# Performance work log

Hardware: AMD Instinct MI355X
Metric: run time of the kernel (lower is better)

The kernel has to match this reference:

```python
import jax, jax.numpy as jnp
import numpy as np

B, T, D, H, L, INNER = 2, 2048, 1024, 16, 8, 4096
EPS = 1e-5
MASK_BIAS = -10000.0

def setup_inputs() -> dict:
    key = jax.random.key(0)
    ks = jax.random.split(key, 6)
    std = 0.02
    w = lambda k, shape: jax.random.normal(k, shape, jnp.float32) * std
    return {
        "inputs_embeds": jax.random.normal(ks[0], (B, T, D), jnp.float32),
        "attention_mask": jnp.ones((B, T), jnp.float32),
        "ln1_w": jnp.ones((L, D), jnp.float32), "ln1_b": jnp.zeros((L, D), jnp.float32),
        "attn_w": w(ks[1], (L, D, 3 * D)), "attn_b": jnp.zeros((L, 3 * D), jnp.float32),
        "proj_w": w(ks[2], (L, D, D)), "proj_b": jnp.zeros((L, D), jnp.float32),
        "ln2_w": jnp.ones((L, D), jnp.float32), "ln2_b": jnp.zeros((L, D), jnp.float32),
        "fc_w": w(ks[3], (L, D, INNER)), "fc_b": jnp.zeros((L, INNER), jnp.float32),
        "fcp_w": w(ks[4], (L, INNER, D)), "fcp_b": jnp.zeros((L, D), jnp.float32),
        "lnf_w": jnp.ones((D,), jnp.float32), "lnf_b": jnp.zeros((D,), jnp.float32),
    }

def _ln(x, w, b):
    m = jnp.mean(x, axis=-1, keepdims=True)
    v = jnp.var(x, axis=-1, keepdims=True)
    return (x - m) * jax.lax.rsqrt(v + EPS) * w + b

def reference(inputs_embeds, attention_mask, ln1_w, ln1_b, attn_w, attn_b,
              proj_w, proj_b, ln2_w, ln2_b, fc_w, fc_b, fcp_w, fcp_b,
              lnf_w, lnf_b):
    hd = D // H
    scale = 1.0 / np.sqrt(hd).astype(np.float32)
    causal = jnp.tril(jnp.ones((T, T), bool))            # [T,T]
    add_mask = (1.0 - attention_mask)[:, None, None, :] * MASK_BIAS  # [B,1,1,T]
    heads = lambda t: t.reshape(B, T, H, hd).transpose(0, 2, 1, 3)   # [B,H,T,hd]
    h = inputs_embeds  # dropout is identity at eval
    for i in range(L):
        # --- causal self-attention (manual QK^T / softmax / AV) ---
        x = _ln(h, ln1_w[i], ln1_b[i])
        qkv = x @ attn_w[i] + attn_b[i]                  # [B,T,3D]
        q, k, v = (heads(t) for t in jnp.split(qkv, 3, axis=-1))
        s = jnp.einsum('bhqd,bhkd->bhqk', q, k) * scale  # [B,H,T,T]
        s = jnp.where(causal, s, MASK_BIAS) + add_mask   # masked_fill then additive mask
        p = jax.nn.softmax(s, axis=-1)
        ctx = jnp.einsum('bhqk,bhkd->bhqd', p, v)
        ctx = ctx.transpose(0, 2, 1, 3).reshape(B, T, D)
        h = h + ctx @ proj_w[i] + proj_b[i]
        # --- feed-forward ---
        x = _ln(h, ln2_w[i], ln2_b[i])
        h = h + jax.nn.relu(x @ fc_w[i] + fc_b[i]) @ fcp_w[i] + fcp_b[i]
    return _ln(h, lnf_w, lnf_b)
```

## Files before the change

### kernel.cpp

```cpp
#include <hip/hip_runtime.h>
#include <math.h>

namespace {
constexpr int kB = 2;
constexpr int kT = 2048;
constexpr int kD = 1024;
constexpr int kH = 16;
constexpr int kL = 8;
constexpr int kInner = 4096;
constexpr int kM = kB * kT;
constexpr float kEps = 1e-5f;
}

typedef __attribute__((ext_vector_type(8))) short bf16x8;
typedef __attribute__((ext_vector_type(4))) float f32x4;
typedef __attribute__((ext_vector_type(16))) float f32x16;

typedef const __attribute__((address_space(1))) void* gas_t;
typedef __attribute__((address_space(3))) void* las_t;

__device__ __forceinline__ short f2bf(float f) {
  union { float f; unsigned u; } v{f};
  unsigned r = (v.u + 0x7FFF + ((v.u >> 16) & 1)) >> 16;
  return (short)r;
}

__device__ __forceinline__ unsigned cvtpk_bf16(float lo, float hi) {
  unsigned r;
  asm("v_cvt_pk_bf16_f32 %0, %1, %2" : "=v"(r) : "v"(lo), "v"(hi));
  return r;
}

__device__ __forceinline__ void half_swap(unsigned& a, unsigned& b, bool ishi) {
  const unsigned sel = ishi ? a : b;
  const unsigned got = (unsigned)__shfl_xor((int)sel, 32, 64);
  a = ishi ? got : a;
  b = ishi ? b : got;
}

template <typename OT>
__global__ __launch_bounds__(256) void ln_kernel(
    const float* __restrict__ in, const float* __restrict__ w,
    const float* __restrict__ b, OT* __restrict__ out) {
  const int row = blockIdx.x;
  const int tid = threadIdx.x;
  const float4 v = ((const float4*)(in + (size_t)row * kD))[tid];
  float sum = v.x + v.y + v.z + v.w;
  float sq = v.x * v.x + v.y * v.y + v.z * v.z + v.w * v.w;
#pragma unroll
  for (int off = 32; off > 0; off >>= 1) {
    sum += __shfl_down(sum, off);
    sq += __shfl_down(sq, off);
  }
  __shared__ float s1[4], s2[4];
  const int wave = tid >> 6, lane = tid & 63;
  if (lane == 0) { s1[wave] = sum; s2[wave] = sq; }
  __syncthreads();
  const float ts = s1[0] + s1[1] + s1[2] + s1[3];
  const float tq = s2[0] + s2[1] + s2[2] + s2[3];
  const float mean = ts * (1.0f / kD);
  const float var = tq * (1.0f / kD) - mean * mean;
  const float rs = rsqrtf(var + kEps);
  const float4 w4 = ((const float4*)w)[tid];
  const float4 b4 = ((const float4*)b)[tid];
  float4 o;
  o.x = (v.x - mean) * rs * w4.x + b4.x;
  o.y = (v.y - mean) * rs * w4.y + b4.y;
  o.z = (v.z - mean) * rs * w4.z + b4.z;
  o.w = (v.w - mean) * rs * w4.w + b4.w;
  if constexpr (sizeof(OT) == 4) {
    ((float4*)(out + (size_t)row * kD))[tid] = o;
  } else {
    short4 s4;
    s4.x = f2bf(o.x); s4.y = f2bf(o.y); s4.z = f2bf(o.z); s4.w = f2bf(o.w);
    ((short4*)(out + (size_t)row * kD))[tid] = s4;
  }
}

__global__ __launch_bounds__(256) void convT_kernel(
    const float* __restrict__ aw, const float* __restrict__ pw,
    const float* __restrict__ fw, const float* __restrict__ gw,
    short* __restrict__ awT, short* __restrict__ pwT,
    short* __restrict__ fwT, short* __restrict__ gwT) {
  __shared__ short t[64][66];
  int b = blockIdx.x;
  const float* src; short* dst; int K, N, tk, tn;
  if (b < 768)       { src = aw; dst = awT; K = 1024; N = 3072; tk = b / 48; tn = b % 48; }
  else if (b < 1024) { b -= 768;  src = pw; dst = pwT; K = 1024; N = 1024; tk = b / 16; tn = b % 16; }
  else if (b < 2048) { b -= 1024; src = fw; dst = fwT; K = 1024; N = 4096; tk = b / 64; tn = b % 64; }
  else               { b -= 2048; src = gw; dst = gwT; K = 4096; N = 1024; tk = b / 16; tn = b % 16; }
  const int k0 = tk * 64, n0 = tn * 64;
  const int tr = threadIdx.x >> 4, tc4 = (threadIdx.x & 15) << 2;
#pragma unroll
  for (int i = 0; i < 4; ++i) {
    const int k = tr + i * 16;
    const float4 v = *(const float4*)(src + (size_t)(k0 + k) * N + n0 + tc4);
    t[k][tc4 + 0] = f2bf(v.x); t[k][tc4 + 1] = f2bf(v.y);
    t[k][tc4 + 2] = f2bf(v.z); t[k][tc4 + 3] = f2bf(v.w);
  }
  __syncthreads();
#pragma unroll
  for (int i = 0; i < 4; ++i) {
    const int n = tr + i * 16;
    short4 o;
    o.x = t[tc4 + 0][n]; o.y = t[tc4 + 1][n];
    o.z = t[tc4 + 2][n]; o.w = t[tc4 + 3][n];
    *(short4*)(dst + (size_t)(n0 + n) * K + k0 + tc4) = o;
  }
}

template <int OUT, bool RELU>
__global__ __launch_bounds__(256, 2) void mfma_gemm3(
    const short* __restrict__ A, const short* __restrict__ BT,
    const float* __restrict__ bias, const float* __restrict__ res,
    void* __restrict__ Cout, int N, int K) {
  __shared__ __align__(16) short As[2][128 * 64];
  __shared__ __align__(16) short Bs[2][128 * 64];
  const int tid = threadIdx.x;
  const int w = tid >> 6, lane = tid & 63;
  const int n16 = lane & 15, quad = lane >> 4;
  const int gridN = N >> 7;
  int bid = blockIdx.x;
  const int nwg = gridDim.x;
  bid = (bid & 7) * (nwg >> 3) + (bid >> 3);
  const int m0 = (bid / gridN) * 128, n0 = (bid % gridN) * 128;
  const int wr = (w >> 1) * 64, wc = (w & 1) * 64;

  const short* Ap = A + (size_t)m0 * K;
  const short* Bp = BT + (size_t)n0 * K;

  f32x4 acc[4][4];
#pragma unroll
  for (int i = 0; i < 4; ++i)
#pragma unroll
    for (int j = 0; j < 4; ++j) acc[i][j] = (f32x4)0.f;

  const int srow = tid >> 3;
  const int schunk = tid & 7;

  auto STAGE = [&](int buf, int k0) {
#pragma unroll
    for (int i = 0; i < 4; ++i) {
      const int r = i * 32 + srow;
      const int cs = (schunk ^ (r & 7)) << 3;
      __builtin_amdgcn_global_load_lds(
          (gas_t)(const void*)(Ap + (size_t)r * K + k0 + cs),
          (las_t)(void*)(As[buf] + (i * 32 + w * 8) * 64), 16, 0, 0);
      __builtin_amdgcn_global_load_lds(
          (gas_t)(const void*)(Bp + (size_t)r * K + k0 + cs),
          (las_t)(void*)(Bs[buf] + (i * 32 + w * 8) * 64), 16, 0, 0);
    }
  };

  STAGE(0, 0);
  __syncthreads();
  int cur = 0;

  for (int k0 = 0; k0 < K; k0 += 64) {
    if (k0 + 64 < K) STAGE(cur ^ 1, k0 + 64);
    const short* as_ = As[cur];
    const short* bs_ = Bs[cur];

    bf16x8 af[4][2], bf[4][2];
#pragma unroll
    for (int i = 0; i < 4; ++i) {
      const int m = wr + i * 16 + n16;
      const int n = wc + i * 16 + n16;
#pragma unroll
      for (int kc = 0; kc < 2; ++kc) {
        af[i][kc] =
            *(const bf16x8*)(as_ + m * 64 + ((((kc << 2) + quad) ^ (m & 7)) << 3));
        bf[i][kc] =
            *(const bf16x8*)(bs_ + n * 64 + ((((kc << 2) + quad) ^ (n & 7)) << 3));
      }
    }
    __builtin_amdgcn_s_setprio(1);
#pragma unroll
    for (int i = 0; i < 4; ++i)
#pragma unroll
      for (int j = 0; j < 4; ++j)
#pragma unroll
        for (int kc = 0; kc < 2; ++kc)
          acc[i][j] = __builtin_amdgcn_mfma_f32_16x16x32_bf16(af[i][kc], bf[j][kc],
                                                              acc[i][j], 0, 0, 0);
    __builtin_amdgcn_s_setprio(0);
    __syncthreads();
    cur ^= 1;
  }

#pragma unroll
  for (int j = 0; j < 4; ++j) {
    const int n = n0 + wc + j * 16 + n16;
    const float bv = bias[n];
#pragma unroll
    for (int i = 0; i < 4; ++i) {
#pragma unroll
      for (int r = 0; r < 4; ++r) {
        const int m = m0 + wr + i * 16 + quad * 4 + r;
        float v = acc[i][j][r] + bv;
        if (OUT == 1) {
          ((float*)Cout)[(size_t)m * N + n] = v + res[(size_t)m * N + n];
        } else {
          if (RELU) v = fmaxf(v, 0.f);
          ((short*)Cout)[(size_t)m * N + n] = f2bf(v);
        }
      }
    }
  }
}

__global__ __launch_bounds__(256) void attn_kernel(
    const short* __restrict__ qkv, const float* __restrict__ amaskp,
    short* __restrict__ ctx) {
  __shared__ __align__(16) short smem[2][8192];

  const int tid = threadIdx.x;
  const int w = tid >> 6;
  const int lane = tid & 63;
  const int l31 = lane & 31;
  const int hi = lane >> 5;
  const int bh = blockIdx.x;
  const int bb = bh >> 4, hh = bh & 15;
  const int qb = gridDim.y - 1 - blockIdx.y;
  const int q0 = qb * 128;
  const int qw0 = q0 + w * 32;

  const short* base  = qkv + (size_t)bb * kT * 3072;
  const short* kbase = base + 1024 + hh * 64;
  const short* vbase = base + 2048 + hh * 64;
  const float* amp   = amaskp + bb * kT;

  bf16x8 qf[4];
  {
    const short* qp = base + (size_t)(qw0 + l31) * 3072 + hh * 64 + hi * 8;
#pragma unroll
    for (int mi = 0; mi < 4; ++mi) qf[mi] = *(const bf16x8*)(qp + mi * 16);
  }

  f32x16 O[2];
  O[0] = (f32x16)0.f;
  O[1] = (f32x16)0.f;
  float m_r = -1e30f, l_r = 0.f;

  const int krow = tid >> 3, kch = tid & 7;
  const int vk4 = tid >> 5, vd16 = (tid >> 3) & 3;
  const int vkin = (tid >> 1) & 3, vdh = tid & 1;
  const int wuni = (tid & 192) * 8;

  const unsigned vs0 = (unsigned)(size_t)(las_t)(void*)(&smem[0][4096]);
  const int g = lane >> 4;
  const unsigned vtr =
      vs0 + (unsigned)((g >> 1) * 1024 + (g & 1) * 128 + (lane & 15) * 8);

  auto STAGE = [&](int buf, int k0) {
    short* ks = &smem[buf][0];
    short* vs = &smem[buf][4096];
#pragma unroll
    for (int r2 = 0; r2 < 2; ++r2) {
      const int rr = r2 * 32 + krow;
      __builtin_amdgcn_global_load_lds(
          (gas_t)(const void*)(kbase + (size_t)(k0 + rr) * 3072 +
                               ((kch ^ (rr & 7)) << 3)),
          (las_t)(void*)(ks + r2 * 2048 + wuni), 16, 0, 0);
      const int key = k0 + r2 * 32 + vk4 * 4 + vkin;
      __builtin_amdgcn_global_load_lds(
          (gas_t)(const void*)(vbase + (size_t)key * 3072 + vd16 * 16 + vdh * 8),
          (las_t)(void*)(vs + r2 * 2048 + wuni), 16, 0, 0);
    }
  };

  const int kend = q0 + 128;
  STAGE(0, 0);
  __syncthreads();
  int cur = 0;

  for (int k0 = 0; k0 < kend; k0 += 64) {
    if (k0 + 64 < kend) STAGE(cur ^ 1, k0 + 64);

    if (k0 <= qw0 + 31) {
      const short* ks = &smem[cur][0];

      f32x16 st[2];
      st[0] = (f32x16)0.f;
      st[1] = (f32x16)0.f;
#pragma unroll
      for (int s = 0; s < 2; ++s) {
        const int row = s * 32 + l31;
        const short* kp = ks + row * 64;
#pragma unroll
        for (int mi = 0; mi < 4; ++mi) {
          const bf16x8 kf =
              *(const bf16x8*)(kp + (((2 * mi + hi) ^ (row & 7)) << 3));
          st[s] = __builtin_amdgcn_mfma_f32_32x32x16_bf16(kf, qf[mi], st[s],
                                                          0, 0, 0);
        }
      }

#pragma unroll
      for (int s = 0; s < 2; ++s) {
        const bool pm = (k0 + 32 * s + 31 > qw0);
#pragma unroll
        for (int rq = 0; rq < 4; ++rq) {
          const int kb_ = k0 + 32 * s + 8 * rq + 4 * hi;
          const float4 a4 = *(const float4*)(amp + kb_);
          const float amv0 = (1.f - a4.x) * -10000.f;
          const float amv1 = (1.f - a4.y) * -10000.f;
          const float amv2 = (1.f - a4.z) * -10000.f;
          const float amv3 = (1.f - a4.w) * -10000.f;
          float v0 = st[s][rq * 4 + 0] * 0.125f;
          float v1 = st[s][rq * 4 + 1] * 0.125f;
          float v2 = st[s][rq * 4 + 2] * 0.125f;
          float v3 = st[s][rq * 4 + 3] * 0.125f;
          if (pm) {
            const int q = qw0 + l31;
            if (kb_ + 0 > q) v0 = -10000.f;
            if (kb_ + 1 > q) v1 = -10000.f;
            if (kb_ + 2 > q) v2 = -10000.f;
            if (kb_ + 3 > q) v3 = -10000.f;
          }
          st[s][rq * 4 + 0] = v0 + amv0;
          st[s][rq * 4 + 1] = v1 + amv1;
          st[s][rq * 4 + 2] = v2 + amv2;
          st[s][rq * 4 + 3] = v3 + amv3;
        }
      }

      float mx = st[0][0];
#pragma unroll
      for (int r = 1; r < 16; ++r) mx = fmaxf(mx, st[0][r]);
#pragma unroll
      for (int r = 0; r < 16; ++r) mx = fmaxf(mx, st[1][r]);
      mx = fmaxf(mx, __shfl_xor(mx, 32, 64));
      const float mn = fmaxf(m_r, mx);
      const float al = __expf(m_r - mn);
      m_r = mn;
      float sum = 0.f;
#pragma unroll
      for (int s = 0; s < 2; ++s)
#pragma unroll
        for (int r = 0; r < 16; ++r) {
          const float p = __expf(st[s][r] - mn);
          st[s][r] = p;
          sum += p;
        }
      sum += __shfl_xor(sum, 32, 64);
      l_r = l_r * al + sum;
#pragma unroll
      for (int r = 0; r < 16; ++r) {
        O[0][r] *= al;
        O[1][r] *= al;
      }

      bf16x8 pf[4];
      const bool ishi = (hi != 0);
#pragma unroll
      for (int s = 0; s < 2; ++s) {
#pragma unroll
        for (int hf = 0; hf < 2; ++hf) {
          unsigned wa = cvtpk_bf16(st[s][8 * hf + 0], st[s][8 * hf + 1]);
          unsigned wc = cvtpk_bf16(st[s][8 * hf + 4], st[s][8 * hf + 5]);
          half_swap(wa, wc, ishi);
          unsigned wb = cvtpk_bf16(st[s][8 * hf + 2], st[s][8 * hf + 3]);
          unsigned wd = cvtpk_bf16(st[s][8 * hf + 6], st[s][8 * hf + 7]);
          half_swap(wb, wd, ishi);
          union { unsigned u[4]; bf16x8 h; } f;
          f.u[0] = wa; f.u[1] = wb; f.u[2] = wc; f.u[3] = wd;
          pf[s * 2 + hf] = f.h;
        }
      }

      unsigned long long tv[16];
      const unsigned vb_ = vtr + (unsigned)(cur << 14);
#pragma unroll
      for (int c = 0; c < 4; ++c)
#pragma unroll
        for (int di = 0; di < 2; ++di) {
          asm volatile("ds_read_b64_tr_b16 %0, %1 offset:%2"
                       : "=v"(tv[(c * 2 + di) * 2 + 0])
                       : "v"(vb_), "n"(c * 2048 + di * 256));
          asm volatile("ds_read_b64_tr_b16 %0, %1 offset:%2"
                       : "=v"(tv[(c * 2 + di) * 2 + 1])
                       : "v"(vb_), "n"(c * 2048 + di * 256 + 512));
        }
      asm volatile("s_waitcnt lgkmcnt(0)" ::: "memory");
      __builtin_amdgcn_sched_barrier(0);
#pragma unroll
      for (int c = 0; c < 4; ++c)
#pragma unroll
        for (int di = 0; di < 2; ++di) {
          union { unsigned long long q[2]; bf16x8 h; } vf_;
          vf_.q[0] = tv[(c * 2 + di) * 2 + 0];
          vf_.q[1] = tv[(c * 2 + di) * 2 + 1];
          O[di] = __builtin_amdgcn_mfma_f32_32x32x16_bf16(vf_.h, pf[c], O[di],
                                                          0, 0, 0);
        }
    }

    __syncthreads();
    cur ^= 1;
  }

  const float inv = 1.f / l_r;
  const size_t tok = (size_t)bb * kT + qw0 + l31;
  short* cp = ctx + tok * 1024 + hh * 64 + 4 * hi;
#pragma unroll
  for (int di = 0; di < 2; ++di)
#pragma unroll
    for (int rq = 0; rq < 4; ++rq) {
      short4 o4;
      o4.x = f2bf(O[di][rq * 4 + 0] * inv);
      o4.y = f2bf(O[di][rq * 4 + 1] * inv);
      o4.z = f2bf(O[di][rq * 4 + 2] * inv);
      o4.w = f2bf(O[di][rq * 4 + 3] * inv);
      *(short4*)(cp + di * 32 + rq * 8) = o4;
    }
}

extern "C" void kernel_launch(void* const* d_in, const int* in_sizes, int n_in,
                              void* d_out, int out_size, void* d_ws, size_t ws_size,
                              hipStream_t stream) {
  const float* emb   = (const float*)d_in[0];
  const float* amask = (const float*)d_in[1];
  const float* ln1w  = (const float*)d_in[2];
  const float* ln1b  = (const float*)d_in[3];
  const float* attnw = (const float*)d_in[4];
  const float* attnb = (const float*)d_in[5];
  const float* projw = (const float*)d_in[6];
  const float* projb = (const float*)d_in[7];
  const float* ln2w  = (const float*)d_in[8];
  const float* ln2b  = (const float*)d_in[9];
  const float* fcw   = (const float*)d_in[10];
  const float* fcb   = (const float*)d_in[11];
  const float* fcpw  = (const float*)d_in[12];
  const float* fcpb  = (const float*)d_in[13];
  const float* lnfw  = (const float*)d_in[14];
  const float* lnfb  = (const float*)d_in[15];
  float* out = (float*)d_out;

  float* h    = (float*)d_ws;
  short* xb   = (short*)(h + (size_t)kM * kD);
  short* ctxb = xb + (size_t)kM * kD;
  short* bigb = ctxb + (size_t)kM * kD;
  short* awT  = bigb + (size_t)kM * kInner;
  short* pwT  = awT + (size_t)3072 * 1024;
  short* fwT  = pwT + (size_t)1024 * 1024;
  short* gwT  = fwT + (size_t)4096 * 1024;

  hipMemcpyAsync(h, emb, sizeof(float) * (size_t)kM * kD,
                 hipMemcpyDeviceToDevice, stream);

  const dim3 blk(256);
  for (int l = 0; l < kL; ++l) {
    convT_kernel<<<3072, blk, 0, stream>>>(
        attnw + (size_t)l * kD * 3072, projw + (size_t)l * kD * kD,
        fcw + (size_t)l * kD * kInner, fcpw + (size_t)l * kInner * kD,
        awT, pwT, fwT, gwT);
    ln_kernel<short><<<kM, blk, 0, stream>>>(h, ln1w + l * kD, ln1b + l * kD, xb);
    mfma_gemm3<0, false><<<(3072 / 128) * (kM / 128), blk, 0, stream>>>(
        xb, awT, attnb + l * 3072, nullptr, bigb, 3072, 1024);
    attn_kernel<<<dim3(kB * kH, kT / 128), blk, 0, stream>>>(bigb, amask, ctxb);
    mfma_gemm3<1, false><<<(1024 / 128) * (kM / 128), blk, 0, stream>>>(
        ctxb, pwT, projb + l * kD, h, h, 1024, 1024);
    ln_kernel<short><<<kM, blk, 0, stream>>>(h, ln2w + l * kD, ln2b + l * kD, xb);
    mfma_gemm3<0, true><<<(4096 / 128) * (kM / 128), blk, 0, stream>>>(
        xb, fwT, fcb + l * kInner, nullptr, bigb, 4096, 1024);
    mfma_gemm3<1, false><<<(1024 / 128) * (kM / 128), blk, 0, stream>>>(
        bigb, gwT, fcpb + l * kD, h, h, 1024, 4096);
  }
  ln_kernel<float><<<kM, blk, 0, stream>>>(h, lnfw, lnfb, out);
}
```

Measured before the change: 2.392 ms.

## Single-buffer GEMM for higher occupancy, narrow N tiles, lazy softmax rescale

The GEMM drops LDS double buffering and raises launch bounds to 4 waves per SIMD, so more blocks can be resident. It also gains a template N-tile width, and the two N=1024 GEMMs now use 64-wide tiles, which doubles their block count. In attention, the online-softmax rescale of the running max, sum and output is skipped when the new block max exceeds the old by no more than 8. This trades load/compute overlap inside a block for occupancy-based latency hiding, and the lazy rescale accepts exponentials bounded by e^8.

```diff
diff --git a/kernel.cpp b/kernel.cpp
--- a/kernel.cpp
+++ b/kernel.cpp
@@ -109,87 +109,81 @@
   }
 }
 
-template <int OUT, bool RELU>
-__global__ __launch_bounds__(256, 2) void mfma_gemm3(
+template <int BN_, int OUT, bool RELU>
+__global__ __launch_bounds__(256, 4) void mfma_gemm3(
     const short* __restrict__ A, const short* __restrict__ BT,
     const float* __restrict__ bias, const float* __restrict__ res,
     void* __restrict__ Cout, int N, int K) {
-  __shared__ __align__(16) short As[2][128 * 64];
-  __shared__ __align__(16) short Bs[2][128 * 64];
+  constexpr int NJ = BN_ / 32;
+  __shared__ __align__(16) short As[128 * 64];
+  __shared__ __align__(16) short Bs[BN_ * 64];
   const int tid = threadIdx.x;
   const int w = tid >> 6, lane = tid & 63;
   const int n16 = lane & 15, quad = lane >> 4;
-  const int gridN = N >> 7;
+  const int gridN = N / BN_;
   int bid = blockIdx.x;
   const int nwg = gridDim.x;
   bid = (bid & 7) * (nwg >> 3) + (bid >> 3);
-  const int m0 = (bid / gridN) * 128, n0 = (bid % gridN) * 128;
-  const int wr = (w >> 1) * 64, wc = (w & 1) * 64;
+  const int m0 = (bid / gridN) * 128, n0 = (bid % gridN) * BN_;
+  const int wr = (w >> 1) * 64, wc = (w & 1) * (BN_ / 2);
 
   const short* Ap = A + (size_t)m0 * K;
   const short* Bp = BT + (size_t)n0 * K;
 
-  f32x4 acc[4][4];
+  f32x4 acc[4][NJ];
 #pragma unroll
   for (int i = 0; i < 4; ++i)
 #pragma unroll
-    for (int j = 0; j < 4; ++j) acc[i][j] = (f32x4)0.f;
+    for (int j = 0; j < NJ; ++j) acc[i][j] = (f32x4)0.f;
 
   const int srow = tid >> 3;
   const int schunk = tid & 7;
 
-  auto STAGE = [&](int buf, int k0) {
+  for (int k0 = 0; k0 < K; k0 += 64) {
 #pragma unroll
     for (int i = 0; i < 4; ++i) {
       const int r = i * 32 + srow;
       const int cs = (schunk ^ (r & 7)) << 3;
       __builtin_amdgcn_global_load_lds(
           (gas_t)(const void*)(Ap + (size_t)r * K + k0 + cs),
-          (las_t)(void*)(As[buf] + (i * 32 + w * 8) * 64), 16, 0, 0);
-      __builtin_amdgcn_global_load_lds(
-          (gas_t)(const void*)(Bp + (size_t)r * K + k0 + cs),
-          (las_t)(void*)(Bs[buf] + (i * 32 + w * 8) * 64), 16, 0, 0);
-    }
-  };
-
-  STAGE(0, 0);
-  __syncthreads();
-  int cur = 0;
-
-  for (int k0 = 0; k0 < K; k0 += 64) {
-    if (k0 + 64 < K) STAGE(cur ^ 1, k0 + 64);
-    const short* as_ = As[cur];
-    const short* bs_ = Bs[cur];
-
-    bf16x8 af[4][2], bf[4][2];
+          (las_t)(void*)(As + (i * 32 + w * 8) * 64), 16, 0, 0);
+      if (i < NJ)
+        __builtin_amdgcn_global_load_lds(
+            (gas_t)(const void*)(Bp + (size_t)r * K + k0 + cs),
+            (las_t)(void*)(Bs + (i * 32 + w * 8) * 64), 16, 0, 0);
+    }
+    __syncthreads();
+
+    bf16x8 af[4][2], bf[NJ][2];
 #pragma unroll
     for (int i = 0; i < 4; ++i) {
       const int m = wr + i * 16 + n16;
-      const int n = wc + i * 16 + n16;
-#pragma unroll
-      for (int kc = 0; kc < 2; ++kc) {
+#pragma unroll
+      for (int kc = 0; kc < 2; ++kc)
         af[i][kc] =
-            *(const bf16x8*)(as_ + m * 64 + ((((kc << 2) + quad) ^ (m & 7)) << 3));
-        bf[i][kc] =
-            *(const bf16x8*)(bs_ + n * 64 + ((((kc << 2) + quad) ^ (n & 7)) << 3));
-      }
-    }
-    __builtin_amdgcn_s_setprio(1);
+            *(const bf16x8*)(As + m * 64 + ((((kc << 2) + quad) ^ (m & 7)) << 3));
+    }
+#pragma unroll
+    for (int j = 0; j < NJ; ++j) {
+      const int n = wc + j * 16 + n16;
+#pragma unroll
+      for (int kc = 0; kc < 2; ++kc)
+        bf[j][kc] =
+            *(const bf16x8*)(Bs + n * 64 + ((((kc << 2) + quad) ^ (n & 7)) << 3));
+    }
 #pragma unroll
     for (int i = 0; i < 4; ++i)
 #pragma unroll
-      for (int j = 0; j < 4; ++j)
+      for (int j = 0; j < NJ; ++j)
 #pragma unroll
         for (int kc = 0; kc < 2; ++kc)
           acc[i][j] = __builtin_amdgcn_mfma_f32_16x16x32_bf16(af[i][kc], bf[j][kc],
                                                               acc[i][j], 0, 0, 0);
-    __builtin_amdgcn_s_setprio(0);
     __syncthreads();
-    cur ^= 1;
-  }
-
-#pragma unroll
-  for (int j = 0; j < 4; ++j) {
+  }
+
+#pragma unroll
+  for (int j = 0; j < NJ; ++j) {
     const int n = n0 + wc + j * 16 + n16;
     const float bv = bias[n];
 #pragma unroll
@@ -331,25 +325,28 @@
 #pragma unroll
       for (int r = 0; r < 16; ++r) mx = fmaxf(mx, st[1][r]);
       mx = fmaxf(mx, __shfl_xor(mx, 32, 64));
-      const float mn = fmaxf(m_r, mx);
-      const float al = __expf(m_r - mn);
-      m_r = mn;
+      if (!__all(mx <= m_r + 8.f)) {
+        const float mn = fmaxf(m_r, mx);
+        const float al = __expf(m_r - mn);
+        m_r = mn;
+        l_r *= al;
+#pragma unroll
+        for (int r = 0; r < 16; ++r) {
+          O[0][r] *= al;
+          O[1][r] *= al;
+        }
+      }
       float sum = 0.f;
 #pragma unroll
       for (int s = 0; s < 2; ++s)
 #pragma unroll
         for (int r = 0; r < 16; ++r) {
-          const float p = __expf(st[s][r] - mn);
+          const float p = __expf(st[s][r] - m_r);
           st[s][r] = p;
           sum += p;
         }
       sum += __shfl_xor(sum, 32, 64);
-      l_r = l_r * al + sum;
-#pragma unroll
-      for (int r = 0; r < 16; ++r) {
-        O[0][r] *= al;
-        O[1][r] *= al;
-      }
+      l_r += sum;
 
       bf16x8 pf[4];
       const bool ishi = (hi != 0);
@@ -456,15 +453,15 @@
         fcw + (size_t)l * kD * kInner, fcpw + (size_t)l * kInner * kD,
         awT, pwT, fwT, gwT);
     ln_kernel<short><<<kM, blk, 0, stream>>>(h, ln1w + l * kD, ln1b + l * kD, xb);
-    mfma_gemm3<0, false><<<(3072 / 128) * (kM / 128), blk, 0, stream>>>(
+    mfma_gemm3<128, 0, false><<<(3072 / 128) * (kM / 128), blk, 0, stream>>>(
         xb, awT, attnb + l * 3072, nullptr, bigb, 3072, 1024);
     attn_kernel<<<dim3(kB * kH, kT / 128), blk, 0, stream>>>(bigb, amask, ctxb);
-    mfma_gemm3<1, false><<<(1024 / 128) * (kM / 128), blk, 0, stream>>>(
+    mfma_gemm3<64, 1, false><<<(1024 / 64) * (kM / 128), blk, 0, stream>>>(
         ctxb, pwT, projb + l * kD, h, h, 1024, 1024);
     ln_kernel<short><<<kM, blk, 0, stream>>>(h, ln2w + l * kD, ln2b + l * kD, xb);
-    mfma_gemm3<0, true><<<(4096 / 128) * (kM / 128), blk, 0, stream>>>(
+    mfma_gemm3<128, 0, true><<<(4096 / 128) * (kM / 128), blk, 0, stream>>>(
         xb, fwT, fcb + l * kInner, nullptr, bigb, 4096, 1024);
-    mfma_gemm3<1, false><<<(1024 / 128) * (kM / 128), blk, 0, stream>>>(
+    mfma_gemm3<64, 1, false><<<(1024 / 64) * (kM / 128), blk, 0, stream>>>(
         bigb, gwT, fcpb + l * kD, h, h, 1024, 4096);
   }
   ln_kernel<float><<<kM, blk, 0, stream>>>(h, lnfw, lnfb, out);
```

Result: faster. 2.296 ms (-4.0%).
